# Optimization experiments

Hardware: AMD Instinct MI355X
Metric: run time of the kernel (lower is better)

The kernel has to match this reference:

```python
import jax, jax.numpy as jnp
import numpy as np

B, S, D = 2, 2048, 4096
NH, NKV = 32, 8
HD = D // NH          # 128
NREP = NH // NKV      # 4 (GQA groups)


def _rope(t, cos, sin):
    # t: [b, s, h, d]; cos/sin: [s, d//2]; interleaved (real, imag) pairs on last dim
    tr = t.reshape(*t.shape[:-1], -1, 2)
    a, b = tr[..., 0], tr[..., 1]
    c = cos[None, :, None, :]
    s = sin[None, :, None, :]
    out = jnp.stack([a * c - b * s, a * s + b * c], axis=-1)
    return out.reshape(t.shape)


def _repeat_kv(t, n_rep):
    # [b, s, n_kv, d] -> [b, s, n_kv*n_rep, d]
    b, s, nkv, d = t.shape
    return jnp.broadcast_to(t[:, :, :, None, :], (b, s, nkv, n_rep, d)).reshape(b, s, nkv * n_rep, d)


def setup_inputs() -> dict:
    key = jax.random.key(0)
    ks = jax.random.split(key, 5)
    x = jax.random.normal(ks[0], (B, S, D), jnp.float32)
    wq = jax.random.normal(ks[1], (D, NH * HD), jnp.float32) * 0.02
    wk = jax.random.normal(ks[2], (D, NKV * HD), jnp.float32) * 0.02
    wv = jax.random.normal(ks[3], (D, NKV * HD), jnp.float32) * 0.02
    wo = jax.random.normal(ks[4], (NH * HD, D), jnp.float32) * 0.02
    inv_freq = 1.0 / (10000.0 ** (jnp.arange(0, HD, 2, dtype=jnp.float32) / HD))
    angles = jnp.arange(S, dtype=jnp.float32)[:, None] * inv_freq[None, :]  # [S, HD//2]
    return {
        "x": x, "wq": wq, "wk": wk, "wv": wv, "wo": wo,
        "freqs_cos": jnp.cos(angles), "freqs_sin": jnp.sin(angles),
        "start_pos": 0,
    }


def reference(x, wq, wk, wv, wo, freqs_cos, freqs_sin, start_pos):
    b, s, _ = x.shape
    xq = (x @ wq).reshape(b, s, NH, HD)
    xk = (x @ wk).reshape(b, s, NKV, HD)
    xv = (x @ wv).reshape(b, s, NKV, HD)
    xq = _rope(xq, freqs_cos, freqs_sin)
    xk = _rope(xk, freqs_cos, freqs_sin)
    # prefill (start_pos=0): cache[:b, :s] = xk/xv, then keys/values read back equal xk/xv
    keys = _repeat_kv(xk, NREP)    # [b, s, NH, HD]
    values = _repeat_kv(xv, NREP)  # [b, s, NH, HD]
    scores = jnp.einsum("bqhd,bkhd->bhqk", xq, keys) / jnp.sqrt(jnp.float32(HD))
    probs = jax.nn.softmax(scores, axis=-1)
    out = jnp.einsum("bhqk,bkhd->bqhd", probs, values).reshape(b, s, NH * HD)
    return out @ wo
```

## Files before the change

kernel.cpp:

```cpp
#include <hip/hip_runtime.h>
#include <hip/hip_bf16.h>
#include <cstdint>

#define B_   2
#define S_   2048
#define D_   4096
#define NH_  32
#define NKV_ 8
#define HD_  128
#define BS_  (B_*S_)
#define NQK_ 6144

typedef __bf16 bf16_t;
typedef __bf16 bf16x8 __attribute__((ext_vector_type(8)));
typedef __bf16 bf16x4 __attribute__((ext_vector_type(4)));
typedef __bf16 bf16x2 __attribute__((ext_vector_type(2)));
typedef float  f32x4  __attribute__((ext_vector_type(4)));
typedef unsigned uint32x4 __attribute__((ext_vector_type(4)));

typedef const __attribute__((address_space(1))) void* gas_ptr;
typedef __attribute__((address_space(3))) void* las_ptr;

__device__ __forceinline__ void gload_lds16(const void* g, void* l) {
  __builtin_amdgcn_global_load_lds((gas_ptr)g, (las_ptr)l, 16, 0, 0);
}

__device__ __forceinline__ float exp2_fast(float x) {
  float r;
  asm("v_exp_f32 %0, %1" : "=v"(r) : "v"(x));
  return r;
}

__device__ __forceinline__ unsigned cvt_pk_bf16(float a, float b) {
  unsigned r;
  asm("v_cvt_pk_bf16_f32 %0, %1, %2" : "=v"(r) : "v"(a), "v"(b));
  return r;
}

#define LD8(p) (*(const bf16x8*)(p))
#define MFMA(a, b, c) __builtin_amdgcn_mfma_f32_16x16x32_bf16(a, b, c, 0, 0, 0)

__global__ __launch_bounds__(256) void k_cvt(const float4* __restrict__ in,
                                             bf16x4* __restrict__ out, int n4) {
  int i = blockIdx.x * 256 + threadIdx.x;
  if (i >= n4) return;
  float4 v = in[i];
  bf16x4 o = { (bf16_t)v.x, (bf16_t)v.y, (bf16_t)v.z, (bf16_t)v.w };
  out[i] = o;
}

__global__ __launch_bounds__(256) void k_transpose_cvt(const float* __restrict__ w,
                                                       bf16_t* __restrict__ wt,
                                                       int K, int N) {
  __shared__ float tile[32][33];
  int n0 = blockIdx.x * 32, k0 = blockIdx.y * 32;
  int tx = threadIdx.x, ty = threadIdx.y;
#pragma unroll
  for (int i = 0; i < 4; i++)
    tile[ty + 8*i][tx] = w[(size_t)(k0 + ty + 8*i) * N + n0 + tx];
  __syncthreads();
#pragma unroll
  for (int i = 0; i < 4; i++)
    wt[(size_t)(n0 + ty + 8*i) * K + k0 + tx] = (bf16_t)tile[tx][ty + 8*i];
}

template <typename CT>
__global__ __launch_bounds__(512, 2) void k_gemm8p(const bf16_t* __restrict__ A,
                                                   const bf16_t* __restrict__ Bt,
                                                   CT* __restrict__ C,
                                                   int M, int N, int K, int KL,
                                                   long long zsC) {
  constexpr int NF = 4;
  __shared__ __align__(16) bf16_t As[2][256 * 64];
  __shared__ __align__(16) bf16_t Bs[2][NF * 64 * 64];
  const int tid = threadIdx.x;
  const int l = tid & 63, w = tid >> 6;
  const int lr = l & 15, lg = l >> 4;
  const int wm = w >> 2, wn = w & 3;

  const int bm = blockIdx.x, bn = blockIdx.y;
  const int kOff = blockIdx.z * KL;

  const bf16_t* Ab = A  + (size_t)bm * 256 * K + kOff;
  const bf16_t* Bb = Bt + (size_t)bn * 256 * K + kOff;
  C += (long long)blockIdx.z * zsC;

  int st_row[4], st_col[4], st_dst[4];
#pragma unroll
  for (int j = 0; j < 4; j++) {
    int o = (j * 512 + tid) * 16;
    int row = o >> 7, cb = o & 127;
    st_row[j] = row;
    st_col[j] = (cb ^ ((row & 7) << 4)) >> 1;
    st_dst[j] = o >> 1;
  }

  int aoff[8], boff[NF];
#pragma unroll
  for (int m = 0; m < 8; m++) {
    int r = wm * 128 + m * 16 + lr;
    aoff[m] = r * 64 + (((lg * 16) ^ ((r & 7) << 4)) >> 1);
  }
#pragma unroll
  for (int n = 0; n < NF; n++) {
    int r = wn * 64 + n * 16 + lr;
    boff[n] = r * 64 + (((lg * 16) ^ ((r & 7) << 4)) >> 1);
  }

  f32x4 acc[8][NF];
#pragma unroll
  for (int m = 0; m < 8; m++)
#pragma unroll
    for (int n = 0; n < NF; n++) acc[m][n] = f32x4{0.f, 0.f, 0.f, 0.f};

  auto stageA = [&](int k, int h) {
    const int kt = k << 6;
    const int rof = h << 7;
#pragma unroll
    for (int j = 0; j < 2; j++)
      gload_lds16(Ab + (size_t)(st_row[j] + rof) * K + kt + st_col[j],
                  &As[k & 1][0] + (rof << 6) + st_dst[j]);
  };
  auto stageB = [&](int k) {
    const int kt = k << 6;
#pragma unroll
    for (int j = 0; j < NF; j++)
      gload_lds16(Bb + (size_t)st_row[j] * K + kt + st_col[j],
                  &Bs[k & 1][0] + st_dst[j]);
  };

  const int NT = KL >> 6;
  stageA(0, 0); stageA(0, 1); stageB(0); stageB(1);
  asm volatile("s_waitcnt vmcnt(4)" ::: "memory");
  __builtin_amdgcn_s_barrier();

  for (int k = 0; k < NT; ++k) {
    const bf16_t* Ap = &As[k & 1][0];
    const bf16_t* Bp = &Bs[k & 1][0];
    const bool s1 = (k + 1 < NT), s2 = (k + 2 < NT);
    bf16x8 bfr[NF], a[4];

#pragma unroll
    for (int n = 0; n < NF; n++) bfr[n] = LD8(Bp + boff[n]);
#pragma unroll
    for (int m = 0; m < 4; m++) a[m] = LD8(Ap + aoff[m]);
    if (s1) stageA(k + 1, 0);
    __builtin_amdgcn_s_barrier();
    asm volatile("s_waitcnt lgkmcnt(0)" ::: "memory");
    __builtin_amdgcn_s_setprio(1);
#pragma unroll
    for (int m = 0; m < 4; m++)
#pragma unroll
      for (int n = 0; n < NF; n++)
        acc[m][n] = MFMA(a[m], bfr[n], acc[m][n]);
    __builtin_amdgcn_s_setprio(0);
    __builtin_amdgcn_s_barrier();

#pragma unroll
    for (int m = 0; m < 4; m++) a[m] = LD8(Ap + aoff[m + 4]);
    if (s1) stageA(k + 1, 1);
    __builtin_amdgcn_s_barrier();
    asm volatile("s_waitcnt lgkmcnt(0)" ::: "memory");
    __builtin_amdgcn_s_setprio(1);
#pragma unroll
    for (int m = 0; m < 4; m++)
#pragma unroll
      for (int n = 0; n < NF; n++)
        acc[m + 4][n] = MFMA(a[m], bfr[n], acc[m + 4][n]);
    __builtin_amdgcn_s_setprio(0);
    __builtin_amdgcn_s_barrier();

#pragma unroll
    for (int n = 0; n < NF; n++) bfr[n] = LD8(Bp + (boff[n] ^ 32));
#pragma unroll
    for (int m = 0; m < 4; m++) a[m] = LD8(Ap + (aoff[m] ^ 32));
    __builtin_amdgcn_s_barrier();
    asm volatile("s_waitcnt lgkmcnt(0)" ::: "memory");
    __builtin_amdgcn_s_setprio(1);
#pragma unroll
    for (int m = 0; m < 4; m++)
#pragma unroll
      for (int n = 0; n < NF; n++)
        acc[m][n] = MFMA(a[m], bfr[n], acc[m][n]);
    __builtin_amdgcn_s_setprio(0);
    __builtin_amdgcn_s_barrier();

#pragma unroll
    for (int m = 0; m < 4; m++) a[m] = LD8(Ap + (aoff[m + 4] ^ 32));
    if (s2) {
      stageB(k + 2);
      asm volatile("s_waitcnt vmcnt(4)" ::: "memory");
    } else if (s1) {
      asm volatile("s_waitcnt vmcnt(0)" ::: "memory");
    }
    __builtin_amdgcn_s_barrier();
    asm volatile("s_waitcnt lgkmcnt(0)" ::: "memory");
    __builtin_amdgcn_s_setprio(1);
#pragma unroll
    for (int m = 0; m < 4; m++)
#pragma unroll
      for (int n = 0; n < NF; n++)
        acc[m + 4][n] = MFMA(a[m], bfr[n], acc[m + 4][n]);
    __builtin_amdgcn_s_setprio(0);
    __builtin_amdgcn_s_barrier();
  }

#pragma unroll
  for (int m = 0; m < 8; m++) {
    int row0 = bm * 256 + wm * 128 + m * 16 + lg * 4;
#pragma unroll
    for (int n = 0; n < NF; n++) {
      int col = bn * 256 + wn * 64 + n * 16 + lr;
#pragma unroll
      for (int i = 0; i < 4; i++)
        C[(size_t)(row0 + i) * N + col] = (CT)acc[m][n][i];
    }
  }
}

__global__ __launch_bounds__(256) void k_rope(const bf16_t* __restrict__ s1,
                                              const bf16_t* __restrict__ s2,
                                              const float* __restrict__ fcos,
                                              const float* __restrict__ fsin,
                                              bf16_t* __restrict__ dst,
                                              int nheads, int stride, float mul) {
  int idx = blockIdx.x * 256 + threadIdx.x;
  int p = idx & 63;
  int h = (idx >> 6) % nheads;
  int bs = idx / (64 * nheads);
  int s = bs & (S_ - 1);
  int b = bs >> 11;
  size_t off = (size_t)bs * stride + h * HD_ + 2 * p;
  bf16x2 ab = *(const bf16x2*)(s1 + off);
  float a = (float)ab[0], bb = (float)ab[1];
  if (s2) {
    bf16x2 ab2 = *(const bf16x2*)(s2 + off);
    a += (float)ab2[0]; bb += (float)ab2[1];
  }
  float c = fcos[s * 64 + p], sn = fsin[s * 64 + p];
  bf16x2 o = { (bf16_t)((a * c - bb * sn) * mul), (bf16_t)((a * sn + bb * c) * mul) };
  *(bf16x2*)(dst + ((((size_t)b * nheads + h) * S_ + s) * HD_) + 2 * p) = o;
}

__global__ __launch_bounds__(256) void k_vtrans(const bf16_t* __restrict__ pA,
                                                const bf16_t* __restrict__ pB,
                                                bf16_t* __restrict__ vtr) {
  __shared__ bf16_t tile[32][33];
  int s0 = blockIdx.x * 32, d0 = blockIdx.y * 32, z = blockIdx.z;
  int b = z >> 3, kvh = z & 7;
  int tx = threadIdx.x, ty = threadIdx.y;
#pragma unroll
  for (int i = 0; i < 4; i++) {
    size_t off = (size_t)(b * S_ + s0 + ty + 8*i) * 2048 + 1024 + kvh * HD_ + d0 + tx;
    tile[ty + 8*i][tx] = (bf16_t)((float)pA[off] + (float)pB[off]);
  }
  __syncthreads();
#pragma unroll
  for (int i = 0; i < 4; i++)
    vtr[((size_t)z * HD_ + d0 + ty + 8*i) * S_ + s0 + tx] = tile[tx][ty + 8*i];
}

#define KVBLK 64
#define SM_THR 12.0f
__global__ __launch_bounds__(256, 2) void k_flash(const bf16_t* __restrict__ qr,
                                                  const bf16_t* __restrict__ kr,
                                                  const bf16_t* __restrict__ vt,
                                                  bf16_t* __restrict__ ctx) {
  __shared__ __align__(16) bf16_t Ks[2][KVBLK * HD_];
  __shared__ __align__(16) bf16_t Vs[2][HD_ * KVBLK];
  const int tid = threadIdx.x;
  const int l = tid & 63, w = tid >> 6;
  const int lr = l & 15, lg = l >> 4;
  const int qb = blockIdx.x, h = blockIdx.y, b = blockIdx.z;
  const int kvh = h >> 2;

  const bf16_t* qbase = qr + (((size_t)b * NH_ + h) * S_ + qb * 128 + w * 32) * HD_;
  const bf16_t* kbase = kr + (((size_t)b * NKV_ + kvh) * S_) * HD_;
  const bf16_t* vbase = vt + (((size_t)b * NKV_ + kvh) * HD_) * S_;

  const int sl0 = (lr + ((lg & 1) << 5)) << 2;
  const int sl1 = sl0 + (16 << 2);

  bf16x8 qf[2][4];
#pragma unroll
  for (int m = 0; m < 2; m++)
#pragma unroll
    for (int kk = 0; kk < 4; kk++)
      qf[m][kk] = *(const bf16x8*)(qbase + (m * 16 + lr) * HD_ + kk * 32 + lg * 8);

  bf16x8 ones;
#pragma unroll
  for (int j = 0; j < 8; j++) ones[j] = (bf16_t)1.0f;

  f32x4 o[2][9];
#pragma unroll
  for (int m = 0; m < 2; m++)
#pragma unroll
    for (int n = 0; n < 9; n++) o[m][n] = f32x4{0.f, 0.f, 0.f, 0.f};
  float mR[2] = {-1e30f, -1e30f};

  auto stage = [&](int bu, int t) {
    const int kb = t * KVBLK;
#pragma unroll
    for (int j = 0; j < 4; j++) {
      int o_ = (tid + 256 * j) * 16;
      int row = o_ >> 8, cb = o_ & 255;
      int scb = cb ^ ((row & 7) << 4);
      gload_lds16(kbase + (size_t)(kb + row) * HD_ + (scb >> 1),
                  &Ks[bu][0] + (o_ >> 1));
    }
#pragma unroll
    for (int j = 0; j < 4; j++) {
      int o_ = (tid + 256 * j) * 16;
      int row = o_ >> 7, cb = o_ & 127;
      int scb = cb ^ ((row & 7) << 4);
      gload_lds16(vbase + (size_t)row * S_ + kb + (scb >> 1),
                  &Vs[bu][0] + (o_ >> 1));
    }
  };

  const int nt = S_ / KVBLK;
  stage(0, 0);
  __syncthreads();
  int buf = 0;

  for (int t = 0; t < nt; t++) {
    if (t + 1 < nt) stage(buf ^ 1, t + 1);
    const bf16_t* Kb = &Ks[buf][0];
    const bf16_t* Vb = &Vs[buf][0];

    f32x4 sc[2][4];
#pragma unroll
    for (int m = 0; m < 2; m++)
#pragma unroll
      for (int n = 0; n < 4; n++) sc[m][n] = f32x4{0.f, 0.f, 0.f, 0.f};
    __builtin_amdgcn_s_setprio(1);
#pragma unroll
    for (int n = 0; n < 4; n++) {
#pragma unroll
      for (int kk = 0; kk < 4; kk++) {
        int r = n * 16 + lr;
        int cb = (kk * 64 + lg * 16) ^ ((r & 7) << 4);
        bf16x8 kf = *(const bf16x8*)(Kb + (((r << 8) + cb) >> 1));
        sc[0][n] = MFMA(kf, qf[0][kk], sc[0][n]);
        sc[1][n] = MFMA(kf, qf[1][kk], sc[1][n]);
      }
    }
    __builtin_amdgcn_s_setprio(0);

    bf16x8 pf[2][2];
#pragma unroll
    for (int m = 0; m < 2; m++) {
      float lm = sc[m][0][0];
#pragma unroll
      for (int n = 0; n < 4; n++)
#pragma unroll
        for (int i = 0; i < 4; i++)
          if (n | i) lm = fmaxf(lm, sc[m][n][i]);
      if (!__all(lm - mR[m] <= SM_THR)) {
        float tmx = fmaxf(lm, __shfl_xor(lm, 16));
        tmx = fmaxf(tmx, __shfl_xor(tmx, 32));
        float mnew = fmaxf(mR[m], tmx);
        float alpha = exp2_fast(mR[m] - mnew);
        mR[m] = mnew;
        float av[4];
#pragma unroll
        for (int i = 0; i < 4; i++) av[i] = __shfl(alpha, lg * 4 + i);
#pragma unroll
        for (int n = 0; n < 9; n++)
#pragma unroll
          for (int i = 0; i < 4; i++) o[m][n][i] *= av[i];
      }
      unsigned W[4][2];
#pragma unroll
      for (int n = 0; n < 4; n++) {
        float p0 = exp2_fast(sc[m][n][0] - mR[m]);
        float p1 = exp2_fast(sc[m][n][1] - mR[m]);
        float p2 = exp2_fast(sc[m][n][2] - mR[m]);
        float p3 = exp2_fast(sc[m][n][3] - mR[m]);
        W[n][0] = cvt_pk_bf16(p0, p1);
        W[n][1] = cvt_pk_bf16(p2, p3);
      }
#pragma unroll
      for (int kk = 0; kk < 2; kk++) {
        uint32x4 wv;
#pragma unroll
        for (int t2 = 0; t2 < 4; t2++) {
          int srcb = (t2 < 2) ? sl0 : sl1;
          unsigned lo = (unsigned)__builtin_amdgcn_ds_bpermute(srcb, (int)W[2 * kk][t2 & 1]);
          unsigned hi = (unsigned)__builtin_amdgcn_ds_bpermute(srcb, (int)W[2 * kk + 1][t2 & 1]);
          wv[t2] = (l & 32) ? hi : lo;
        }
        pf[m][kk] = __builtin_bit_cast(bf16x8, wv);
      }
    }

    __builtin_amdgcn_s_setprio(1);
#pragma unroll
    for (int n = 0; n < 8; n++) {
#pragma unroll
      for (int kk = 0; kk < 2; kk++) {
        int r = n * 16 + lr;
        int cb = (kk * 64 + lg * 16) ^ ((r & 7) << 4);
        bf16x8 vf = *(const bf16x8*)(Vb + (((r << 7) + cb) >> 1));
        o[0][n] = MFMA(pf[0][kk], vf, o[0][n]);
        o[1][n] = MFMA(pf[1][kk], vf, o[1][n]);
      }
    }
    o[0][8] = MFMA(pf[0][0], ones, o[0][8]);
    o[0][8] = MFMA(pf[0][1], ones, o[0][8]);
    o[1][8] = MFMA(pf[1][0], ones, o[1][8]);
    o[1][8] = MFMA(pf[1][1], ones, o[1][8]);
    __builtin_amdgcn_s_setprio(0);
    __syncthreads();
    buf ^= 1;
  }

#pragma unroll
  for (int m = 0; m < 2; m++)
#pragma unroll
    for (int i = 0; i < 4; i++) {
      float inv = 1.0f / o[m][8][i];
      int srow = qb * 128 + w * 32 + m * 16 + lg * 4 + i;
#pragma unroll
      for (int n = 0; n < 8; n++) {
        int d = n * 16 + lr;
        ctx[((size_t)(b * S_ + srow)) * D_ + h * HD_ + d] = (bf16_t)(o[m][n][i] * inv);
      }
    }
}

extern "C" void kernel_launch(void* const* d_in, const int* in_sizes, int n_in,
                              void* d_out, int out_size, void* d_ws, size_t ws_size,
                              hipStream_t stream) {
  const float* x    = (const float*)d_in[0];
  const float* wq   = (const float*)d_in[1];
  const float* wk   = (const float*)d_in[2];
  const float* wv   = (const float*)d_in[3];
  const float* wo   = (const float*)d_in[4];
  const float* fcos = (const float*)d_in[5];
  const float* fsin = (const float*)d_in[6];
  float* out = (float*)d_out;

  const size_t MB = 1u << 20;
  char* p = (char*)d_ws;
  bf16_t* xb    = (bf16_t*)p;
  bf16_t* wqkvt = (bf16_t*)(p + 32 * MB);
  bf16_t* wot   = (bf16_t*)(p + 80 * MB);
  bf16_t* qc    = (bf16_t*)(p + 112 * MB);
  bf16_t* partA = (bf16_t*)(p + 144 * MB);
  bf16_t* partB = wot;
  bf16_t* qrope = xb;
  bf16_t* krope = wqkvt;
  bf16_t* vtr   = wqkvt + (size_t)BS_ * NKV_ * HD_;
  bf16_t* ctx   = qc;

  const float QSCALE = (float)(0.08838834764831845 * 1.4426950408889634);

  dim3 tb(32, 8);
  k_cvt<<<BS_ * D_ / 1024, 256, 0, stream>>>((const float4*)x, (bf16x4*)xb, BS_ * D_ / 4);
  k_transpose_cvt<<<dim3(D_ / 32, D_ / 32), tb, 0, stream>>>(wq, wqkvt, D_, D_);
  k_transpose_cvt<<<dim3(32, D_ / 32), tb, 0, stream>>>(wk, wqkvt + (size_t)D_ * D_, D_, NKV_ * HD_);
  k_transpose_cvt<<<dim3(32, D_ / 32), tb, 0, stream>>>(wv, wqkvt + (size_t)(D_ + NKV_ * HD_) * D_, D_, NKV_ * HD_);
  k_gemm8p<bf16_t><<<dim3(BS_ / 256, D_ / 256, 1), 512, 0, stream>>>(
      xb, wqkvt, qc, BS_, D_, D_, D_, 0);
  k_gemm8p<bf16_t><<<dim3(BS_ / 256, 2048 / 256, 2), 512, 0, stream>>>(
      xb, wqkvt + (size_t)D_ * D_, partA, BS_, 2048, D_, 2048,
      (long long)(partB - partA));
  k_rope<<<BS_ * NH_ * 64 / 256, 256, 0, stream>>>(qc, (const bf16_t*)nullptr,
      fcos, fsin, qrope, NH_, D_, QSCALE);
  k_rope<<<BS_ * NKV_ * 64 / 256, 256, 0, stream>>>(partA, partB,
      fcos, fsin, krope, NKV_, 2048, 1.0f);
  k_vtrans<<<dim3(S_ / 32, HD_ / 32, B_ * NKV_), tb, 0, stream>>>(partA, partB, vtr);
  k_transpose_cvt<<<dim3(D_ / 32, D_ / 32), tb, 0, stream>>>(wo, wot, D_, D_);
  k_flash<<<dim3(S_ / 128, NH_, B_), 256, 0, stream>>>(qrope, krope, vtr, ctx);
  k_gemm8p<float><<<dim3(BS_ / 256, D_ / 256, 1), 512, 0, stream>>>(
      ctx, wot, out, BS_, D_, D_, D_, 0);
}
```

Baseline: 575.1 us.

## Switch flash attention to 32x32x16 MFMA with permlane P repack and LDS-staged output

Rewrites the flash-attention inner loop to use 32x32x16 bf16 MFMA tiles instead of 16x16x32, so each wave covers 32 queries in a single tile. It replaces the ds_bpermute reshuffle of P with v_permlane32_swap and computes the row sum with scalar adds instead of an extra MFMA against a ones vector. The epilogue stages normalized output through LDS so ctx is written with 16-byte vector stores. This should cut LDS traffic, MFMA instruction count and scattered global stores. The cost is a different register footprint and an added barrier before the store.

```diff
diff --git a/kernel.cpp b/kernel.cpp
--- a/kernel.cpp
+++ b/kernel.cpp
@@ -16,6 +16,7 @@
 typedef __bf16 bf16x4 __attribute__((ext_vector_type(4)));
 typedef __bf16 bf16x2 __attribute__((ext_vector_type(2)));
 typedef float  f32x4  __attribute__((ext_vector_type(4)));
+typedef float  f32x16 __attribute__((ext_vector_type(16)));
 typedef unsigned uint32x4 __attribute__((ext_vector_type(4)));
 
 typedef const __attribute__((address_space(1))) void* gas_ptr;
@@ -39,6 +40,7 @@
 
 #define LD8(p) (*(const bf16x8*)(p))
 #define MFMA(a, b, c) __builtin_amdgcn_mfma_f32_16x16x32_bf16(a, b, c, 0, 0, 0)
+#define MFMA32(a, b, c) __builtin_amdgcn_mfma_f32_32x32x16_bf16(a, b, c, 0, 0, 0)
 
 __global__ __launch_bounds__(256) void k_cvt(const float4* __restrict__ in,
                                              bf16x4* __restrict__ out, int n4) {
@@ -270,34 +272,25 @@
   __shared__ __align__(16) bf16_t Vs[2][HD_ * KVBLK];
   const int tid = threadIdx.x;
   const int l = tid & 63, w = tid >> 6;
-  const int lr = l & 15, lg = l >> 4;
-  const int qb = blockIdx.x, h = blockIdx.y, b = blockIdx.z;
-  const int kvh = h >> 2;
-
-  const bf16_t* qbase = qr + (((size_t)b * NH_ + h) * S_ + qb * 128 + w * 32) * HD_;
+  const int q5 = l & 31, h = l >> 5;
+  const int qb = blockIdx.x, hh = blockIdx.y, b = blockIdx.z;
+  const int kvh = hh >> 2;
+
+  const bf16_t* qbase = qr + (((size_t)b * NH_ + hh) * S_ + qb * 128 + w * 32) * HD_;
   const bf16_t* kbase = kr + (((size_t)b * NKV_ + kvh) * S_) * HD_;
   const bf16_t* vbase = vt + (((size_t)b * NKV_ + kvh) * HD_) * S_;
 
-  const int sl0 = (lr + ((lg & 1) << 5)) << 2;
-  const int sl1 = sl0 + (16 << 2);
-
-  bf16x8 qf[2][4];
-#pragma unroll
-  for (int m = 0; m < 2; m++)
-#pragma unroll
-    for (int kk = 0; kk < 4; kk++)
-      qf[m][kk] = *(const bf16x8*)(qbase + (m * 16 + lr) * HD_ + kk * 32 + lg * 8);
-
-  bf16x8 ones;
-#pragma unroll
-  for (int j = 0; j < 8; j++) ones[j] = (bf16_t)1.0f;
-
-  f32x4 o[2][9];
-#pragma unroll
-  for (int m = 0; m < 2; m++)
-#pragma unroll
-    for (int n = 0; n < 9; n++) o[m][n] = f32x4{0.f, 0.f, 0.f, 0.f};
-  float mR[2] = {-1e30f, -1e30f};
+  bf16x8 qf[8];
+#pragma unroll
+  for (int s = 0; s < 8; s++)
+    qf[s] = LD8(qbase + q5 * HD_ + s * 16 + h * 8);
+
+  f32x16 acco[4];
+#pragma unroll
+  for (int db = 0; db < 4; db++)
+#pragma unroll
+    for (int r = 0; r < 16; r++) acco[db][r] = 0.f;
+  float mR = -1e30f, lR = 0.f;
 
   auto stage = [&](int bu, int t) {
     const int kb = t * KVBLK;
@@ -329,105 +322,103 @@
     const bf16_t* Kb = &Ks[buf][0];
     const bf16_t* Vb = &Vs[buf][0];
 
-    f32x4 sc[2][4];
-#pragma unroll
-    for (int m = 0; m < 2; m++)
-#pragma unroll
-      for (int n = 0; n < 4; n++) sc[m][n] = f32x4{0.f, 0.f, 0.f, 0.f};
-    __builtin_amdgcn_s_setprio(1);
-#pragma unroll
-    for (int n = 0; n < 4; n++) {
-#pragma unroll
-      for (int kk = 0; kk < 4; kk++) {
-        int r = n * 16 + lr;
-        int cb = (kk * 64 + lg * 16) ^ ((r & 7) << 4);
-        bf16x8 kf = *(const bf16x8*)(Kb + (((r << 8) + cb) >> 1));
-        sc[0][n] = MFMA(kf, qf[0][kk], sc[0][n]);
-        sc[1][n] = MFMA(kf, qf[1][kk], sc[1][n]);
+    f32x16 accs[2];
+#pragma unroll
+    for (int kb = 0; kb < 2; kb++)
+#pragma unroll
+      for (int r = 0; r < 16; r++) accs[kb][r] = 0.f;
+    __builtin_amdgcn_s_setprio(1);
+#pragma unroll
+    for (int s = 0; s < 8; s++) {
+#pragma unroll
+      for (int kb = 0; kb < 2; kb++) {
+        int r = kb * 32 + q5;
+        int cb = (32 * s + 16 * h) ^ ((r & 7) << 4);
+        bf16x8 kf = LD8(Kb + (r << 7) + (cb >> 1));
+        accs[kb] = MFMA32(kf, qf[s], accs[kb]);
       }
     }
     __builtin_amdgcn_s_setprio(0);
 
-    bf16x8 pf[2][2];
-#pragma unroll
-    for (int m = 0; m < 2; m++) {
-      float lm = sc[m][0][0];
-#pragma unroll
-      for (int n = 0; n < 4; n++)
-#pragma unroll
-        for (int i = 0; i < 4; i++)
-          if (n | i) lm = fmaxf(lm, sc[m][n][i]);
-      if (!__all(lm - mR[m] <= SM_THR)) {
-        float tmx = fmaxf(lm, __shfl_xor(lm, 16));
-        tmx = fmaxf(tmx, __shfl_xor(tmx, 32));
-        float mnew = fmaxf(mR[m], tmx);
-        float alpha = exp2_fast(mR[m] - mnew);
-        mR[m] = mnew;
-        float av[4];
-#pragma unroll
-        for (int i = 0; i < 4; i++) av[i] = __shfl(alpha, lg * 4 + i);
-#pragma unroll
-        for (int n = 0; n < 9; n++)
-#pragma unroll
-          for (int i = 0; i < 4; i++) o[m][n][i] *= av[i];
+    float lm = accs[0][0];
+#pragma unroll
+    for (int kb = 0; kb < 2; kb++)
+#pragma unroll
+      for (int r = 0; r < 16; r++)
+        if (kb | r) lm = fmaxf(lm, accs[kb][r]);
+    if (!__all(lm - mR <= SM_THR)) {
+      float fm = fmaxf(lm, __shfl_xor(lm, 32));
+      float mnew = fmaxf(mR, fm);
+      float alpha = exp2_fast(mR - mnew);
+      mR = mnew;
+      lR *= alpha;
+#pragma unroll
+      for (int db = 0; db < 4; db++)
+#pragma unroll
+        for (int r = 0; r < 16; r++) acco[db][r] *= alpha;
+    }
+    float psum = 0.f;
+    bf16x8 pb[4];
+#pragma unroll
+    for (int s2 = 0; s2 < 4; s2++) {
+      const int kb = s2 >> 1, rb = (s2 & 1) * 8;
+      float pv[8];
+#pragma unroll
+      for (int j = 0; j < 8; j++) {
+        pv[j] = exp2_fast(accs[kb][rb + j] - mR);
+        psum += pv[j];
       }
-      unsigned W[4][2];
-#pragma unroll
-      for (int n = 0; n < 4; n++) {
-        float p0 = exp2_fast(sc[m][n][0] - mR[m]);
-        float p1 = exp2_fast(sc[m][n][1] - mR[m]);
-        float p2 = exp2_fast(sc[m][n][2] - mR[m]);
-        float p3 = exp2_fast(sc[m][n][3] - mR[m]);
-        W[n][0] = cvt_pk_bf16(p0, p1);
-        W[n][1] = cvt_pk_bf16(p2, p3);
+      unsigned wlo0 = cvt_pk_bf16(pv[0], pv[1]);
+      unsigned wlo1 = cvt_pk_bf16(pv[2], pv[3]);
+      unsigned whi0 = cvt_pk_bf16(pv[4], pv[5]);
+      unsigned whi1 = cvt_pk_bf16(pv[6], pv[7]);
+      asm volatile("v_permlane32_swap_b32 %0, %1" : "+v"(wlo0), "+v"(whi0));
+      asm volatile("v_permlane32_swap_b32 %0, %1" : "+v"(wlo1), "+v"(whi1));
+      uint32x4 wv = { wlo0, wlo1, whi0, whi1 };
+      pb[s2] = __builtin_bit_cast(bf16x8, wv);
+    }
+    psum += __shfl_xor(psum, 32);
+    lR += psum;
+
+    __builtin_amdgcn_s_setprio(1);
+#pragma unroll
+    for (int s2 = 0; s2 < 4; s2++) {
+#pragma unroll
+      for (int db = 0; db < 4; db++) {
+        int rv = db * 32 + q5;
+        int cb = (32 * s2 + 16 * h) ^ ((rv & 7) << 4);
+        bf16x8 vf = LD8(Vb + (rv << 6) + (cb >> 1));
+        acco[db] = MFMA32(vf, pb[s2], acco[db]);
       }
-#pragma unroll
-      for (int kk = 0; kk < 2; kk++) {
-        uint32x4 wv;
-#pragma unroll
-        for (int t2 = 0; t2 < 4; t2++) {
-          int srcb = (t2 < 2) ? sl0 : sl1;
-          unsigned lo = (unsigned)__builtin_amdgcn_ds_bpermute(srcb, (int)W[2 * kk][t2 & 1]);
-          unsigned hi = (unsigned)__builtin_amdgcn_ds_bpermute(srcb, (int)W[2 * kk + 1][t2 & 1]);
-          wv[t2] = (l & 32) ? hi : lo;
-        }
-        pf[m][kk] = __builtin_bit_cast(bf16x8, wv);
-      }
-    }
-
-    __builtin_amdgcn_s_setprio(1);
-#pragma unroll
-    for (int n = 0; n < 8; n++) {
-#pragma unroll
-      for (int kk = 0; kk < 2; kk++) {
-        int r = n * 16 + lr;
-        int cb = (kk * 64 + lg * 16) ^ ((r & 7) << 4);
-        bf16x8 vf = *(const bf16x8*)(Vb + (((r << 7) + cb) >> 1));
-        o[0][n] = MFMA(pf[0][kk], vf, o[0][n]);
-        o[1][n] = MFMA(pf[1][kk], vf, o[1][n]);
-      }
-    }
-    o[0][8] = MFMA(pf[0][0], ones, o[0][8]);
-    o[0][8] = MFMA(pf[0][1], ones, o[0][8]);
-    o[1][8] = MFMA(pf[1][0], ones, o[1][8]);
-    o[1][8] = MFMA(pf[1][1], ones, o[1][8]);
+    }
     __builtin_amdgcn_s_setprio(0);
     __syncthreads();
     buf ^= 1;
   }
 
-#pragma unroll
-  for (int m = 0; m < 2; m++)
-#pragma unroll
-    for (int i = 0; i < 4; i++) {
-      float inv = 1.0f / o[m][8][i];
-      int srow = qb * 128 + w * 32 + m * 16 + lg * 4 + i;
-#pragma unroll
-      for (int n = 0; n < 8; n++) {
-        int d = n * 16 + lr;
-        ctx[((size_t)(b * S_ + srow)) * D_ + h * HD_ + d] = (bf16_t)(o[m][n][i] * inv);
-      }
-    }
+  float inv = 1.0f / lR;
+  bf16_t* tb = &Ks[0][0] + w * (32 * 128);
+#pragma unroll
+  for (int db = 0; db < 4; db++)
+#pragma unroll
+    for (int rp = 0; rp < 8; rp++) {
+      int r = 2 * rp;
+      int d0 = (r & 3) + 8 * (r >> 2) + 4 * h + 32 * db;
+      unsigned word = cvt_pk_bf16(acco[db][r] * inv, acco[db][r + 1] * inv);
+      int cbyte = (d0 * 2) ^ ((q5 & 7) << 4);
+      *(unsigned*)((char*)tb + q5 * 256 + cbyte) = word;
+    }
+  __syncthreads();
+#pragma unroll
+  for (int it = 0; it < 8; it++) {
+    int gid = it * 256 + tid;
+    int wv = gid >> 9, rem = gid & 511;
+    int qq = rem >> 4, g = rem & 15;
+    int cbyte = (g * 16) ^ ((qq & 7) << 4);
+    bf16x8 v = LD8((const bf16_t*)((const char*)(&Ks[0][0] + wv * (32 * 128)) + qq * 256 + cbyte));
+    int srow = qb * 128 + wv * 32 + qq;
+    *(bf16x8*)(ctx + ((size_t)(b * S_ + srow)) * D_ + hh * HD_ + g * 8) = v;
+  }
 }
 
 extern "C" void kernel_launch(void* const* d_in, const int* in_sizes, int n_in,
```

New measurement: 569.2 us. Within noise of the previous version (-1.0%).
